# Performance work log

Hardware: AMD Instinct MI355X
Metric: run time of the kernel (lower is better)

The kernel has to match this reference:

```python
import jax, jax.numpy as jnp
import numpy as np

H = 256

def setup_inputs() -> dict:
    key = jax.random.key(0)
    ks = jax.random.split(key, 8)
    B, S = 32, 4096
    hidden = jax.random.normal(ks[0], (B, H), dtype=jnp.float32)
    encoder_outputs = jax.random.normal(ks[1], (B, S, H), dtype=jnp.float32)
    scale = 1.0 / np.sqrt(H)
    W1_w = jax.random.uniform(ks[2], (H, H), jnp.float32, -scale, scale)
    W1_b = jax.random.uniform(ks[3], (H,), jnp.float32, -scale, scale)
    W2_w = jax.random.uniform(ks[4], (H, H), jnp.float32, -scale, scale)
    W2_b = jax.random.uniform(ks[5], (H,), jnp.float32, -scale, scale)
    V_w = jax.random.uniform(ks[6], (H, 1), jnp.float32, -scale, scale)
    V_b = jax.random.uniform(ks[7], (1,), jnp.float32, -scale, scale)
    return {"hidden": hidden, "encoder_outputs": encoder_outputs,
            "W1_w": W1_w, "W1_b": W1_b, "W2_w": W2_w, "W2_b": W2_b,
            "V_w": V_w, "V_b": V_b}

def reference(hidden, encoder_outputs, W1_w, W1_b, W2_w, W2_b, V_w, V_b):
    # hidden: (B,H), encoder_outputs: (B,S,H)
    q = hidden @ W1_w + W1_b                     # (B,H)
    k = jnp.einsum('bsh,hd->bsd', encoder_outputs, W2_w) + W2_b  # (B,S,H)
    energy = jnp.tanh(q[:, None, :] + k)         # (B,S,H)
    scores = jnp.einsum('bsh,ho->bso', energy, V_w) + V_b        # (B,S,1)
    attention_weights = jax.nn.softmax(scores, axis=1)           # (B,S,1)
    context_vector = jnp.einsum('bso,bsh->bh', attention_weights, encoder_outputs)  # (B,H)
    return attention_weights, context_vector
```

## Files before the change

### kernel.cpp

```cpp
#include <hip/hip_runtime.h>
#include <hip/hip_bf16.h>
#include <math.h>

#define BB 32
#define SS 4096
#define HH 256

typedef __bf16 bf16x8 __attribute__((ext_vector_type(8)));
typedef float f32x4 __attribute__((ext_vector_type(4)));

#define GLOBAL_AS __attribute__((address_space(1)))
#define LDS_AS    __attribute__((address_space(3)))

__device__ inline bf16x8 cvt8(const float4& x, const float4& y) {
    union { __hip_bfloat162 p[4]; bf16x8 v; } u;
    u.p[0] = __float22bfloat162_rn(make_float2(x.x, x.y));
    u.p[1] = __float22bfloat162_rn(make_float2(x.z, x.w));
    u.p[2] = __float22bfloat162_rn(make_float2(y.x, y.y));
    u.p[3] = __float22bfloat162_rn(make_float2(y.z, y.w));
    return u.v;
}

__device__ inline float fast_tanh(float x) {
    float e = __builtin_amdgcn_exp2f(x * 2.8853900817779268f);
    return 1.f - 2.f * __builtin_amdgcn_rcpf(e + 1.f);
}

__global__ void prep_kernel(const float* __restrict__ W2_w,
                            ushort* __restrict__ w2sw,
                            const float* __restrict__ hidden,
                            const float* __restrict__ W1_w,
                            const float* __restrict__ W1_b,
                            const float* __restrict__ W2_b,
                            const float* __restrict__ V_w,
                            float* __restrict__ qq,
                            float* __restrict__ Mout) {
    __shared__ float red[HH];
    const int t = threadIdx.x;
    if (blockIdx.x < 256) {
        const int i = blockIdx.x * 256 + t;
        const int j    = i & 7;
        const int lane = (i >> 3) & 63;
        const int nt   = (i >> 9) & 15;
        const int kc   = i >> 13;
        const int k = kc * 32 + ((lane >> 4) & 3) * 8 + j;
        const int n = nt * 16 + (lane & 15);
        __hip_bfloat16 h = __float2bfloat16(W2_w[k * HH + n]);
        w2sw[i] = *(ushort*)&h;
    } else if (blockIdx.x < 256 + BB) {
        const int b = blockIdx.x - 256;
        red[t] = hidden[b * HH + t];
        __syncthreads();
        float acc = 0.f;
#pragma unroll 16
        for (int k = 0; k < HH; ++k)
            acc = fmaf(red[k], W1_w[k * HH + t], acc);
        qq[b * HH + t] = acc + W1_b[t] + W2_b[t];
    } else {
        red[t] = fabsf(V_w[t]);
        __syncthreads();
        for (int off = 128; off > 0; off >>= 1) {
            if (t < off) red[t] += red[t + off];
            __syncthreads();
        }
        if (t == 0) Mout[0] = red[0];
    }
}

__global__ __launch_bounds__(1024, 4)
void score_ctx_kernel(const float* __restrict__ enc,
                      const ushort* __restrict__ w2sw,
                      const float* __restrict__ qq,
                      const float* __restrict__ V_w,
                      const float* __restrict__ Mptr,
                      float* __restrict__ wtilde,
                      float* __restrict__ part) {
    extern __shared__ char smem[];
    ushort* w2buf = (ushort*)smem;
    float*  sc    = (float*)(smem + 131072);
    float*  ctxl  = (float*)(smem + 133120);

    const int t    = threadIdx.x;
    const int b    = blockIdx.y;
    const int cx   = blockIdx.x;
    const int wid  = t >> 6;
    const int lane = t & 63;
    const int l15  = lane & 15;
    const int quad = lane >> 4;
    const int mw   = wid & 7;
    const int nw   = wid >> 3;

    {
        const char* gsrc = (const char*)w2sw + t * 16;
        char* ldst = smem + wid * 1024;
#pragma unroll
        for (int i = 0; i < 8; ++i)
            __builtin_amdgcn_global_load_lds(
                (const GLOBAL_AS void*)(gsrc + i * 16384),
                (LDS_AS void*)(ldst + i * 16384), 16, 0, 0);
    }

    const float Mv = Mptr[0];
    float4 cacc = make_float4(0.f, 0.f, 0.f, 0.f);

    __syncthreads();

    for (int p = 0; p < 4; ++p) {
        const int par  = p & 1;
        const int srow = cx * 512 + p * 128 + mw * 16;
        const float* rowp =
            enc + ((size_t)(b * SS + srow + l15)) * HH + (quad << 3);

        f32x4 acc[8];
#pragma unroll
        for (int nt = 0; nt < 8; ++nt) acc[nt] = (f32x4)0.f;

        float4 a0x = *(const float4*)rowp;
        float4 a0y = *(const float4*)(rowp + 4);
#pragma unroll
        for (int kc = 0; kc < 8; ++kc) {
            float4 a1x, a1y;
            if (kc < 7) {
                a1x = *(const float4*)(rowp + (kc + 1) * 32);
                a1y = *(const float4*)(rowp + (kc + 1) * 32 + 4);
            }
            const bf16x8 af = cvt8(a0x, a0y);
#pragma unroll
            for (int nt = 0; nt < 8; ++nt) {
                const bf16x8 bfr = *(const bf16x8*)
                    &w2buf[((kc * 16 + nw * 8 + nt) * 64 + lane) * 8];
                acc[nt] = __builtin_amdgcn_mfma_f32_16x16x32_bf16(
                    af, bfr, acc[nt], 0, 0, 0);
            }
            if (kc < 7) { a0x = a1x; a0y = a1y; }
        }

        float p0[4] = {0.f, 0.f, 0.f, 0.f};
#pragma unroll
        for (int nt = 0; nt < 8; ++nt) {
            const int n = nw * 128 + nt * 16 + l15;
            const float qn = qq[b * HH + n];
            const float vn = V_w[n];
#pragma unroll
            for (int r = 0; r < 4; ++r)
                p0[r] = fmaf(vn, fast_tanh(qn + acc[nt][r]), p0[r]);
        }
#pragma unroll
        for (int off = 1; off < 16; off <<= 1)
#pragma unroll
            for (int r = 0; r < 4; ++r)
                p0[r] += __shfl_xor(p0[r], off);

        if (l15 == 0)
            *(float4*)&sc[(par * 2 + nw) * 128 + mw * 16 + quad * 4] =
                make_float4(p0[0], p0[1], p0[2], p0[3]);
        __syncthreads();

        if (nw == 0 && l15 == 0) {
            const float* o = &sc[(par * 2 + 1) * 128 + mw * 16 + quad * 4];
            *(float4*)&wtilde[(size_t)b * SS + srow + quad * 4] =
                make_float4(__expf(p0[0] + o[0] - Mv),
                            __expf(p0[1] + o[1] - Mv),
                            __expf(p0[2] + o[2] - Mv),
                            __expf(p0[3] + o[3] - Mv));
        }

        const float* ep =
            enc + ((size_t)(b * SS + srow + nw * 8)) * HH + (lane << 2);
        const float* s0p = &sc[(par * 2 + 0) * 128 + mw * 16 + nw * 8];
        const float* s1p = &sc[(par * 2 + 1) * 128 + mw * 16 + nw * 8];
#pragma unroll
        for (int jj = 0; jj < 8; ++jj) {
            const float w = __expf(s0p[jj] + s1p[jj] - Mv);
            const float4 e = *(const float4*)(ep + (size_t)jj * HH);
            cacc.x = fmaf(w, e.x, cacc.x);
            cacc.y = fmaf(w, e.y, cacc.y);
            cacc.z = fmaf(w, e.z, cacc.z);
            cacc.w = fmaf(w, e.w, cacc.w);
        }
    }

    *(float4*)&ctxl[wid * HH + (lane << 2)] = cacc;
    __syncthreads();
    if (t < HH) {
        float s = 0.f;
#pragma unroll
        for (int w = 0; w < 16; ++w) s += ctxl[w * HH + t];
        part[((size_t)(b * 8 + cx)) * HH + t] = s;
    }
}

__global__ __launch_bounds__(256)
void finish_kernel(const float* __restrict__ wtilde,
                   const float* __restrict__ part,
                   float* __restrict__ weights_out,
                   float* __restrict__ ctx_out) {
    __shared__ float red[256];
    __shared__ float linv_s;
    const int b = blockIdx.x;
    const int t = threadIdx.x;

    const float4* wt4 = (const float4*)(wtilde + (size_t)b * SS);
    float4 vals[4];
    float l = 0.f;
#pragma unroll
    for (int i = 0; i < 4; ++i) {
        vals[i] = wt4[i * 256 + t];
        l += vals[i].x + vals[i].y + vals[i].z + vals[i].w;
    }
    red[t] = l;
    __syncthreads();
    for (int off = 128; off > 0; off >>= 1) {
        if (t < off) red[t] += red[t + off];
        __syncthreads();
    }
    if (t == 0) linv_s = 1.f / red[0];
    __syncthreads();
    const float linv = linv_s;

    float4* wo4 = (float4*)(weights_out + (size_t)b * SS);
#pragma unroll
    for (int i = 0; i < 4; ++i) {
        const float4 v = vals[i];
        wo4[i * 256 + t] =
            make_float4(v.x * linv, v.y * linv, v.z * linv, v.w * linv);
    }

    float a = 0.f;
#pragma unroll
    for (int c = 0; c < 8; ++c)
        a += part[((size_t)(b * 8 + c)) * HH + t];
    ctx_out[b * HH + t] = a * linv;
}

extern "C" void kernel_launch(void* const* d_in, const int* in_sizes, int n_in,
                              void* d_out, int out_size, void* d_ws, size_t ws_size,
                              hipStream_t stream) {
    const float* hidden = (const float*)d_in[0];
    const float* enc    = (const float*)d_in[1];
    const float* W1_w   = (const float*)d_in[2];
    const float* W1_b   = (const float*)d_in[3];
    const float* W2_w   = (const float*)d_in[4];
    const float* W2_b   = (const float*)d_in[5];
    const float* V_w    = (const float*)d_in[6];
    const float* V_b    = (const float*)d_in[7];
    (void)V_b;

    float* out_weights = (float*)d_out;
    float* out_ctx     = (float*)d_out + BB * SS;

    float* ws      = (float*)d_ws;
    float* ws_qq   = ws;
    float* ws_wt   = ws_qq + BB * HH;
    float* ws_part = ws_wt + BB * SS;
    float* ws_M    = ws_part + BB * 64 * HH;
    ushort* ws_w2  = (ushort*)(ws_M + 4);

    static bool attr_done = false;
    if (!attr_done) {
        hipFuncSetAttribute(reinterpret_cast<const void*>(score_ctx_kernel),
                            hipFuncAttributeMaxDynamicSharedMemorySize,
                            149504);
        attr_done = true;
    }

    prep_kernel<<<dim3(256 + BB + 1), dim3(256), 0, stream>>>(
        W2_w, ws_w2, hidden, W1_w, W1_b, W2_b, V_w, ws_qq, ws_M);
    score_ctx_kernel<<<dim3(SS / 512, BB), dim3(1024), 149504, stream>>>(
        enc, ws_w2, ws_qq, V_w, ws_M, ws_wt, ws_part);
    finish_kernel<<<dim3(BB), dim3(256), 0, stream>>>(
        ws_wt, ws_part, out_weights, out_ctx);
}
```

Before: 239.2 us.

## Process two M-tiles per wave to reuse W2 fragments and halve pass count

Each wave now computes two 16-row MFMA tiles per pass, so every W2 fragment read from LDS feeds two MFMAs. The loop drops from four passes of 128 rows to two passes of 256 rows, which halves the number of block barriers. The first encoder loads for the second pass are issued right after the barrier, overlapping them with the softmax-weight and context work. The cost is more accumulator registers, which can lower occupancy, and a larger LDS score buffer.

```diff
diff --git a/kernel.cpp b/kernel.cpp
--- a/kernel.cpp
+++ b/kernel.cpp
@@ -78,7 +78,7 @@
     extern __shared__ char smem[];
     ushort* w2buf = (ushort*)smem;
     float*  sc    = (float*)(smem + 131072);
-    float*  ctxl  = (float*)(smem + 133120);
+    float*  ctxl  = (float*)(smem + 139264);
 
     const int t    = threadIdx.x;
     const int b    = blockIdx.y;
@@ -101,78 +101,111 @@
     }
 
     const float Mv = Mptr[0];
+    const size_t encb = (size_t)b * SS;
     float4 cacc = make_float4(0.f, 0.f, 0.f, 0.f);
 
+    const float* rowp0 =
+        enc + (encb + cx * 512 + mw * 32 + l15) * HH + (quad << 3);
+    const float* rowp1 = rowp0 + (size_t)16 * HH;
+    float4 ax0 = *(const float4*)rowp0, ay0 = *(const float4*)(rowp0 + 4);
+    float4 ax1 = *(const float4*)rowp1, ay1 = *(const float4*)(rowp1 + 4);
+
     __syncthreads();
 
-    for (int p = 0; p < 4; ++p) {
-        const int par  = p & 1;
-        const int srow = cx * 512 + p * 128 + mw * 16;
-        const float* rowp =
-            enc + ((size_t)(b * SS + srow + l15)) * HH + (quad << 3);
-
-        f32x4 acc[8];
-#pragma unroll
-        for (int nt = 0; nt < 8; ++nt) acc[nt] = (f32x4)0.f;
-
-        float4 a0x = *(const float4*)rowp;
-        float4 a0y = *(const float4*)(rowp + 4);
+#pragma unroll
+    for (int p = 0; p < 2; ++p) {
+        const int par     = p & 1;
+        const int rowbase = mw * 32;
+        const int srow    = cx * 512 + p * 256 + rowbase;
+
+        f32x4 acc[2][8];
+#pragma unroll
+        for (int mt = 0; mt < 2; ++mt)
+#pragma unroll
+            for (int nt = 0; nt < 8; ++nt) acc[mt][nt] = (f32x4)0.f;
+
 #pragma unroll
         for (int kc = 0; kc < 8; ++kc) {
-            float4 a1x, a1y;
+            float4 n0x, n0y, n1x, n1y;
             if (kc < 7) {
-                a1x = *(const float4*)(rowp + (kc + 1) * 32);
-                a1y = *(const float4*)(rowp + (kc + 1) * 32 + 4);
+                const int o = (kc + 1) * 32;
+                n0x = *(const float4*)(rowp0 + o);
+                n0y = *(const float4*)(rowp0 + o + 4);
+                n1x = *(const float4*)(rowp1 + o);
+                n1y = *(const float4*)(rowp1 + o + 4);
             }
-            const bf16x8 af = cvt8(a0x, a0y);
+            const bf16x8 af0 = cvt8(ax0, ay0);
+            const bf16x8 af1 = cvt8(ax1, ay1);
 #pragma unroll
             for (int nt = 0; nt < 8; ++nt) {
                 const bf16x8 bfr = *(const bf16x8*)
                     &w2buf[((kc * 16 + nw * 8 + nt) * 64 + lane) * 8];
-                acc[nt] = __builtin_amdgcn_mfma_f32_16x16x32_bf16(
-                    af, bfr, acc[nt], 0, 0, 0);
+                acc[0][nt] = __builtin_amdgcn_mfma_f32_16x16x32_bf16(
+                    af0, bfr, acc[0][nt], 0, 0, 0);
+                acc[1][nt] = __builtin_amdgcn_mfma_f32_16x16x32_bf16(
+                    af1, bfr, acc[1][nt], 0, 0, 0);
             }
-            if (kc < 7) { a0x = a1x; a0y = a1y; }
-        }
-
-        float p0[4] = {0.f, 0.f, 0.f, 0.f};
+            if (kc < 7) { ax0 = n0x; ay0 = n0y; ax1 = n1x; ay1 = n1y; }
+        }
+
+        float p0[2][4] = {{0.f, 0.f, 0.f, 0.f}, {0.f, 0.f, 0.f, 0.f}};
 #pragma unroll
         for (int nt = 0; nt < 8; ++nt) {
             const int n = nw * 128 + nt * 16 + l15;
             const float qn = qq[b * HH + n];
             const float vn = V_w[n];
 #pragma unroll
-            for (int r = 0; r < 4; ++r)
-                p0[r] = fmaf(vn, fast_tanh(qn + acc[nt][r]), p0[r]);
+            for (int mt = 0; mt < 2; ++mt)
+#pragma unroll
+                for (int r = 0; r < 4; ++r)
+                    p0[mt][r] =
+                        fmaf(vn, fast_tanh(qn + acc[mt][nt][r]), p0[mt][r]);
         }
 #pragma unroll
         for (int off = 1; off < 16; off <<= 1)
 #pragma unroll
-            for (int r = 0; r < 4; ++r)
-                p0[r] += __shfl_xor(p0[r], off);
-
-        if (l15 == 0)
-            *(float4*)&sc[(par * 2 + nw) * 128 + mw * 16 + quad * 4] =
-                make_float4(p0[0], p0[1], p0[2], p0[3]);
+            for (int mt = 0; mt < 2; ++mt)
+#pragma unroll
+                for (int r = 0; r < 4; ++r)
+                    p0[mt][r] += __shfl_xor(p0[mt][r], off);
+
+        if (l15 == 0) {
+#pragma unroll
+            for (int mt = 0; mt < 2; ++mt)
+                *(float4*)&sc[(par * 2 + nw) * 256 + rowbase + mt * 16 +
+                              quad * 4] =
+                    make_float4(p0[mt][0], p0[mt][1], p0[mt][2], p0[mt][3]);
+        }
         __syncthreads();
 
+        if (p == 0) {
+            rowp0 = enc + (encb + cx * 512 + 256 + mw * 32 + l15) * HH +
+                    (quad << 3);
+            rowp1 = rowp0 + (size_t)16 * HH;
+            ax0 = *(const float4*)rowp0; ay0 = *(const float4*)(rowp0 + 4);
+            ax1 = *(const float4*)rowp1; ay1 = *(const float4*)(rowp1 + 4);
+        }
+
         if (nw == 0 && l15 == 0) {
-            const float* o = &sc[(par * 2 + 1) * 128 + mw * 16 + quad * 4];
-            *(float4*)&wtilde[(size_t)b * SS + srow + quad * 4] =
-                make_float4(__expf(p0[0] + o[0] - Mv),
-                            __expf(p0[1] + o[1] - Mv),
-                            __expf(p0[2] + o[2] - Mv),
-                            __expf(p0[3] + o[3] - Mv));
-        }
-
-        const float* ep =
-            enc + ((size_t)(b * SS + srow + nw * 8)) * HH + (lane << 2);
-        const float* s0p = &sc[(par * 2 + 0) * 128 + mw * 16 + nw * 8];
-        const float* s1p = &sc[(par * 2 + 1) * 128 + mw * 16 + nw * 8];
-#pragma unroll
-        for (int jj = 0; jj < 8; ++jj) {
-            const float w = __expf(s0p[jj] + s1p[jj] - Mv);
-            const float4 e = *(const float4*)(ep + (size_t)jj * HH);
+#pragma unroll
+            for (int mt = 0; mt < 2; ++mt) {
+                const float* o =
+                    &sc[(par * 2 + 1) * 256 + rowbase + mt * 16 + quad * 4];
+                *(float4*)&wtilde[encb + srow + mt * 16 + quad * 4] =
+                    make_float4(__expf(p0[mt][0] + o[0] - Mv),
+                                __expf(p0[mt][1] + o[1] - Mv),
+                                __expf(p0[mt][2] + o[2] - Mv),
+                                __expf(p0[mt][3] + o[3] - Mv));
+            }
+        }
+
+        const float* ep = enc + (encb + srow + nw * 16) * HH + (lane << 2);
+        const float* sA = &sc[(par * 2 + 0) * 256 + rowbase + nw * 16];
+        const float* sB = &sc[(par * 2 + 1) * 256 + rowbase + nw * 16];
+#pragma unroll
+        for (int j = 0; j < 16; ++j) {
+            const float w = __expf(sA[j] + sB[j] - Mv);
+            const float4 e = *(const float4*)(ep + (size_t)j * HH);
             cacc.x = fmaf(w, e.x, cacc.x);
             cacc.y = fmaf(w, e.y, cacc.y);
             cacc.z = fmaf(w, e.z, cacc.z);
@@ -260,13 +293,13 @@
     if (!attr_done) {
         hipFuncSetAttribute(reinterpret_cast<const void*>(score_ctx_kernel),
                             hipFuncAttributeMaxDynamicSharedMemorySize,
-                            149504);
+                            155648);
         attr_done = true;
     }
 
     prep_kernel<<<dim3(256 + BB + 1), dim3(256), 0, stream>>>(
         W2_w, ws_w2, hidden, W1_w, W1_b, W2_b, V_w, ws_qq, ws_M);
-    score_ctx_kernel<<<dim3(SS / 512, BB), dim3(1024), 149504, stream>>>(
+    score_ctx_kernel<<<dim3(SS / 512, BB), dim3(1024), 155648, stream>>>(
         enc, ws_w2, ws_qq, V_w, ws_M, ws_wt, ws_part);
     finish_kernel<<<dim3(BB), dim3(256), 0, stream>>>(
         ws_wt, ws_part, out_weights, out_ctx);
```

Measured after the change: 271.9 us. 1.14x slower.
